# Performance work log

Measured on AMD Instinct MI355X. Metric: run time of the kernel, lower is better.

The kernel has to match this reference:

```python
import jax, jax.numpy as jnp
import numpy as np

N_NODES = 50000
N_EDGES = 600000
D = 128
LN_EPS = 1e-5


def setup_inputs() -> dict:
    key = jax.random.key(0)
    ks = jax.random.split(key, 10)
    s = 1.0 / np.sqrt(D)
    return {
        "node_reps": jax.random.normal(ks[0], (N_NODES, D), jnp.float32),
        "edge_reps": jax.random.normal(ks[1], (N_EDGES, D), jnp.float32),
        "src_idx": jax.random.randint(ks[2], (N_EDGES,), 0, N_NODES, jnp.int32),
        "dst_idx": jnp.sort(jax.random.randint(ks[3], (N_EDGES,), 0, N_NODES, jnp.int32)),
        "Wq": jax.random.normal(ks[4], (D, D), jnp.float32) * s,
        "Wk": jax.random.normal(ks[5], (D, D), jnp.float32) * s,
        "Wv": jax.random.normal(ks[6], (D, D), jnp.float32) * s,
        "Wo": jax.random.normal(ks[7], (D, D), jnp.float32) * s,
        "ln_gamma": jnp.ones((D,), jnp.float32),
        "ln_beta": jnp.zeros((D,), jnp.float32),
        "W1": jax.random.normal(ks[8], (3 * D, D), jnp.float32) * (1.0 / np.sqrt(3 * D)),
        "b1": jnp.zeros((D,), jnp.float32),
        "W2": jax.random.normal(ks[9], (D, D), jnp.float32) * s,
        "b2": jnp.zeros((D,), jnp.float32),
    }


def _layer_norm(x, g, b):
    mu = jnp.mean(x, axis=-1, keepdims=True)
    var = jnp.mean(jnp.square(x - mu), axis=-1, keepdims=True)
    return (x - mu) * jax.lax.rsqrt(var + LN_EPS) * g + b


def reference(node_reps, edge_reps, src_idx, dst_idx, Wq, Wk, Wv, Wo,
              ln_gamma, ln_beta, W1, b1, W2, b2):
    n_nodes, d = node_reps.shape
    # dense projections once per node (kernel-friendly GEMMs)
    q = node_reps @ Wq                                  # [N, d]
    k_nodes = node_reps @ Wk                            # [N, d]
    v_nodes = node_reps @ Wv                            # [N, d]
    # per-edge gather + edge bias
    k_e = k_nodes[src_idx] + edge_reps                  # [E, d]
    scores = jnp.sum(q[dst_idx] * k_e, axis=-1) / jnp.sqrt(jnp.float32(d))  # [E]
    # segment softmax over edges sharing the same dst node
    seg_max = jax.ops.segment_max(scores, dst_idx, num_segments=n_nodes)
    ex = jnp.exp(scores - seg_max[dst_idx])
    denom = jax.ops.segment_sum(ex, dst_idx, num_segments=n_nodes)
    alpha = ex / denom[dst_idx]                          # [E]
    v_e = v_nodes[src_idx] + edge_reps                   # [E, d]
    agg = jax.ops.segment_sum(alpha[:, None] * v_e, dst_idx, num_segments=n_nodes)  # [N, d]
    updated = _layer_norm(node_reps + agg @ Wo, ln_gamma, ln_beta)  # [N, d]
    # triplet fusion MLP over (dst node, edge, src node)
    h_trip = jnp.concatenate([node_reps[dst_idx], edge_reps, node_reps[src_idx]], axis=-1)  # [E, 3d]
    fused = jax.nn.relu(h_trip @ W1 + b1) @ W2 + b2      # [E, d]
    return updated, fused
```

## Files before the change

kernel.cpp:

```cpp
#include <hip/hip_runtime.h>
#include <hip/hip_bf16.h>

#define NN 50000
#define NE 600000
#define D 128

typedef __bf16 bf16x8 __attribute__((ext_vector_type(8)));
typedef __bf16 bf16x4 __attribute__((ext_vector_type(4)));
typedef float f32x4 __attribute__((ext_vector_type(4)));


static __device__ __forceinline__ void gload_lds16(const void* g, void* l) {
  __builtin_amdgcn_global_load_lds(
      (const __attribute__((address_space(1))) unsigned int*)g,
      (__attribute__((address_space(3))) unsigned int*)l, 16, 0, 0);
}

static __device__ __forceinline__ bf16x8 load_a_frag_nc(const float* __restrict__ A,
                                                        int row, int k0) {
  const f32x4* p = (const f32x4*)(A + (size_t)row * D + k0);
  f32x4 v0 = p[0], v1 = p[1];
  bf16x8 r;
  r[0] = (__bf16)v0[0]; r[1] = (__bf16)v0[1]; r[2] = (__bf16)v0[2]; r[3] = (__bf16)v0[3];
  r[4] = (__bf16)v1[0]; r[5] = (__bf16)v1[1]; r[6] = (__bf16)v1[2]; r[7] = (__bf16)v1[3];
  return r;
}

static __device__ __forceinline__ void stage_a_tile64(const float* __restrict__ A, int M,
                                                      int row_base, char* lds, int tid) {
  const int l32 = tid & 31;
  const int g = tid >> 5;
#pragma unroll
  for (int it = 0; it < 8; ++it) {
    int rl = it * 8 + g;
    int r = row_base + rl;
    f32x4 v = {};
    if (r < M) v = *(const f32x4*)(A + (size_t)r * D + l32 * 4);
    bf16x4 b;
    b[0] = (__bf16)v[0]; b[1] = (__bf16)v[1]; b[2] = (__bf16)v[2]; b[3] = (__bf16)v[3];
    int byte = (rl * 256 + l32 * 8) ^ ((rl & 7) << 4);
    *(bf16x4*)(lds + byte) = b;
  }
}

static __device__ __forceinline__ bf16x8 read_a_frag(const char* lds, int rl, int k0) {
  int byte = (rl * 256 + k0 * 2) ^ ((rl & 7) << 4);
  return *(const bf16x8*)(lds + byte);
}

template <int CTRL>
static __device__ __forceinline__ float dpp_add(float x) {
  int v = __builtin_amdgcn_update_dpp(0, __float_as_int(x), CTRL, 0xf, 0xf, true);
  return x + __int_as_float(v);
}

static __device__ __forceinline__ float red32(float x) {
  x = dpp_add<0xB1>(x);
  x = dpp_add<0x4E>(x);
  x = dpp_add<0x124>(x);
  x = dpp_add<0x128>(x);
  return x + __shfl_xor(x, 16, 64);
}

struct PrepArgs {
  const float* W[8];
  __bf16* WT[8];
  const int* dst;
  int* offs;
};

__global__ void prep_all(PrepArgs pa) {
  int b = blockIdx.x;
  if (b < 512) {
    int w = b >> 6;
    int t = (b & 63) * 256 + threadIdx.x;
    int n = t & 127, k = t >> 7;
    pa.WT[w][n * 128 + k] = (__bf16)pa.W[w][k * 128 + n];
  } else {
    int n = (b - 512) * 256 + threadIdx.x;
    if (n > NN) return;
    int lo = 0, hi = NE;
    while (lo < hi) {
      int mid = (lo + hi) >> 1;
      if (pa.dst[mid] < n) lo = mid + 1; else hi = mid;
    }
    pa.offs[n] = lo;
  }
}

struct GemmBatch {
  const __bf16* BT[5];
  void* C[5];
  const float* bias[5];
  int mode[5];
};

__global__ __launch_bounds__(256) void gemm_k128_b(const float* __restrict__ A,
                                                   GemmBatch gb, int M) {
  __shared__ __align__(16) char atile[64 * 256];
  const int tid = threadIdx.x;
  const int lane = tid & 63;
  const int wave = tid >> 6;
  const int wr = wave >> 1, wc = wave & 1;
  const int row0 = blockIdx.x * 64;
  const int col0 = wc * 64;
  const int lr = lane & 15;
  const int lk = (lane >> 4) << 3;
  const int rr = (lane >> 4) * 4;

  stage_a_tile64(A, M, row0, atile, tid);
  __syncthreads();

#pragma unroll
  for (int y = 0; y < 5; ++y) {
    const __bf16* __restrict__ BT = gb.BT[y];
    f32x4 acc[2][4] = {};
#pragma unroll
    for (int kk = 0; kk < 4; ++kk) {
      const int k0 = kk * 32 + lk;
      bf16x8 a[2], b[4];
#pragma unroll
      for (int m = 0; m < 2; ++m) a[m] = read_a_frag(atile, wr * 32 + m * 16 + lr, k0);
#pragma unroll
      for (int n = 0; n < 4; ++n) b[n] = *(const bf16x8*)(BT + (size_t)(col0 + n * 16 + lr) * D + k0);
#pragma unroll
      for (int m = 0; m < 2; ++m)
#pragma unroll
        for (int n = 0; n < 4; ++n)
          acc[m][n] = __builtin_amdgcn_mfma_f32_16x16x32_bf16(a[m], b[n], acc[m][n], 0, 0, 0);
    }
    float bv[4] = {0.f, 0.f, 0.f, 0.f};
    if (gb.bias[y]) {
#pragma unroll
      for (int n = 0; n < 4; ++n) bv[n] = gb.bias[y][col0 + n * 16 + lr];
    }
    const int mode = gb.mode[y];
#pragma unroll
    for (int m = 0; m < 2; ++m)
#pragma unroll
      for (int j = 0; j < 4; ++j) {
        const int r = row0 + wr * 32 + m * 16 + rr + j;
        if (r < M) {
#pragma unroll
          for (int n = 0; n < 4; ++n) {
            const int c = col0 + n * 16 + lr;
            const float val = acc[m][n][j] + bv[n];
            if (mode == 0) {
              ((float*)gb.C[y])[(size_t)r * D + c] = val;
            } else if (mode == 1) {
              ((__bf16*)gb.C[y])[(size_t)r * D + c] = (__bf16)val;
            } else if (mode == 2) {
              ((__bf16*)gb.C[y])[(size_t)r * 256 + c] = (__bf16)val;
            } else {
              ((__bf16*)gb.C[y])[(size_t)r * 256 + 128 + c] = (__bf16)val;
            }
          }
        }
      }
  }
}

#define LD1(P, K, J, SV)                                                     \
  do {                                                                       \
    const int jj_ = (J);                                                     \
    const int jc_ = jj_ < jm ? jj_ : 0;                                      \
    int si_ = __shfl((SV), jj_ & 31, 32);                                    \
    si_ = jj_ < jm ? si_ : 0;                                                \
    kb##P[K] = *(const bf16x4*)(KV + (size_t)si_ * 256 + (l32 << 2));        \
    vb##P[K] = *(const bf16x4*)(KV + (size_t)si_ * 256 + 128 + (l32 << 2));  \
    eb##P[K] = *(const f32x4*)(edge + (size_t)(s0 + jc_) * D + (l32 << 2));  \
  } while (0)

#define LOADC(P, C)                                                          \
  do {                                                                       \
    const int c4_ = (C) * 4;                                                 \
    const int sv_ = (c4_ < 32) ? sidx0 : sidx1;                              \
    LD1(P, 0, c4_ + 0, sv_); LD1(P, 1, c4_ + 1, sv_);                        \
    LD1(P, 2, c4_ + 2, sv_); LD1(P, 3, c4_ + 3, sv_);                        \
  } while (0)

#define CP1(P, K, J)                                                         \
  do {                                                                       \
    const int jj_ = (J);                                                     \
    f32x4 ef_ = eb##P[K];                                                    \
    float x0_ = (float)kb##P[K][0] + ef_[0];                                 \
    float x1_ = (float)kb##P[K][1] + ef_[1];                                 \
    float x2_ = (float)kb##P[K][2] + ef_[2];                                 \
    float x3_ = (float)kb##P[K][3] + ef_[3];                                 \
    float pp_ = fmaf(qs[1], x1_, qs[0] * x0_) + fmaf(qs[3], x3_, qs[2] * x2_); \
    float s_ = red32(pp_);                                                   \
    float w_ = jj_ < jm ? exp2f(s_) : 0.f;                                   \
    l += w_;                                                                 \
    a[0] = fmaf(w_, (float)vb##P[K][0] + ef_[0], a[0]);                      \
    a[1] = fmaf(w_, (float)vb##P[K][1] + ef_[1], a[1]);                      \
    a[2] = fmaf(w_, (float)vb##P[K][2] + ef_[2], a[2]);                      \
    a[3] = fmaf(w_, (float)vb##P[K][3] + ef_[3], a[3]);                      \
  } while (0)

#define COMPC(P, C)                                                          \
  do {                                                                       \
    const int cc4_ = (C) * 4;                                                \
    CP1(P, 0, cc4_ + 0); CP1(P, 1, cc4_ + 1);                                \
    CP1(P, 2, cc4_ + 2); CP1(P, 3, cc4_ + 3);                                \
  } while (0)

__global__ __launch_bounds__(256) __attribute__((amdgpu_waves_per_eu(3)))
void fused_edge_attn(
    const float* __restrict__ edge,
    const __bf16* __restrict__ W1bT,
    const __bf16* __restrict__ W2T,
    const __bf16* __restrict__ P1,
    const __bf16* __restrict__ P3,
    const int* __restrict__ dst,
    const int* __restrict__ src,
    const float* __restrict__ b2,
    float* __restrict__ out_fused,
    const float* __restrict__ Q,
    const __bf16* __restrict__ KV,
    const int* __restrict__ offs,
    const __bf16* __restrict__ WoT,
    const float* __restrict__ noderep,
    const float* __restrict__ gamma,
    const float* __restrict__ beta,
    float* __restrict__ out_updated) {
  __shared__ __align__(16) char bufA[64 * 256];
  __shared__ __align__(16) char bufB[64 * 256];
  const int tid = threadIdx.x;
  const int grp = blockIdx.x / 5;
  const int role = blockIdx.x % 5;

  if (role >= 2) {
    const int ebi = grp * 3 + (role - 2);
    const int eb = ebi * 64;
    const int lane = tid & 63;
    const int wave = tid >> 6;
    const int wr = wave >> 1, wc = wave & 1;
    const int lr = lane & 15;
    const int lk = (lane >> 4) << 3;
    const int col0 = wc * 64;

    {
      const int gr = lane >> 4;
      const int slot = lane & 15;
      int di[4], sg[4];
#pragma unroll
      for (int c = 0; c < 4; ++c) {
        int rl = wave * 16 + c * 4 + gr;
        di[c] = dst[eb + rl];
        sg[c] = src[eb + rl];
      }
#pragma unroll
      for (int c = 0; c < 4; ++c) {
        int rl = wave * 16 + c * 4 + gr;
        int sb = (slot * 16) ^ ((rl & 7) << 4);
        gload_lds16((const char*)(P1 + (size_t)di[c] * D) + sb,
                    bufA + (wave * 16 + c * 4) * 256);
        gload_lds16((const char*)(P3 + (size_t)sg[c] * D) + sb,
                    bufB + (wave * 16 + c * 4) * 256);
      }
    }

    f32x4 acc[2][4] = {};
#pragma unroll
    for (int kk = 0; kk < 4; ++kk) {
      const int k0 = kk * 32 + lk;
      bf16x8 a[2], b[4];
#pragma unroll
      for (int m = 0; m < 2; ++m) a[m] = load_a_frag_nc(edge, eb + wr * 32 + m * 16 + lr, k0);
#pragma unroll
      for (int n = 0; n < 4; ++n) b[n] = *(const bf16x8*)(W1bT + (size_t)(col0 + n * 16 + lr) * D + k0);
#pragma unroll
      for (int m = 0; m < 2; ++m)
#pragma unroll
        for (int n = 0; n < 4; ++n)
          acc[m][n] = __builtin_amdgcn_mfma_f32_16x16x32_bf16(a[m], b[n], acc[m][n], 0, 0, 0);
    }
    __syncthreads();

    const int rr = (lane >> 4) * 4;
#pragma unroll
    for (int m = 0; m < 2; ++m) {
#pragma unroll
      for (int j = 0; j < 4; ++j) {
        int rl = wr * 32 + m * 16 + rr + j;
#pragma unroll
        for (int n = 0; n < 4; ++n) {
          int c = col0 + n * 16 + lr;
          int byte = (rl * 256 + c * 2) ^ ((rl & 7) << 4);
          float g1 = (float)*(const __bf16*)(bufA + byte);
          float g3 = (float)*(const __bf16*)(bufB + byte);
          float v = fmaxf(acc[m][n][j] + g1 + g3, 0.f);
          *(__bf16*)(bufA + byte) = (__bf16)v;
        }
      }
    }
    __syncthreads();

    float b2v[4];
#pragma unroll
    for (int n = 0; n < 4; ++n) b2v[n] = b2[col0 + n * 16 + lr];
    f32x4 acc2[2][4] = {};
#pragma unroll
    for (int kk = 0; kk < 4; ++kk) {
      const int k0 = kk * 32 + lk;
      bf16x8 a[2], b[4];
#pragma unroll
      for (int m = 0; m < 2; ++m) a[m] = read_a_frag(bufA, wr * 32 + m * 16 + lr, k0);
#pragma unroll
      for (int n = 0; n < 4; ++n) b[n] = *(const bf16x8*)(W2T + (size_t)(col0 + n * 16 + lr) * D + k0);
#pragma unroll
      for (int m = 0; m < 2; ++m)
#pragma unroll
        for (int n = 0; n < 4; ++n)
          acc2[m][n] = __builtin_amdgcn_mfma_f32_16x16x32_bf16(a[m], b[n], acc2[m][n], 0, 0, 0);
    }
#pragma unroll
    for (int m = 0; m < 2; ++m)
#pragma unroll
      for (int j = 0; j < 4; ++j) {
        int rl = wr * 32 + m * 16 + rr + j;
        int e = eb + rl;
#pragma unroll
        for (int n = 0; n < 4; ++n) {
          int c = col0 + n * 16 + lr;
          out_fused[(size_t)e * D + c] = acc2[m][n][j] + b2v[n];
        }
      }
  } else {
    const int nw = tid >> 5;
    const int node = (grp * 2 + role) * 8 + nw;
    const int l32 = tid & 31;
    int s0 = offs[node], s1 = offs[node + 1];
    int cnt = s1 - s0;
    f32x4 q = *(const f32x4*)(Q + (size_t)node * D + l32 * 4);
    f32x4 qs;
    qs[0] = q[0] * 0.12751744f; qs[1] = q[1] * 0.12751744f;
    qs[2] = q[2] * 0.12751744f; qs[3] = q[3] * 0.12751744f;
    float l = 0.f;
    f32x4 a = {0.f, 0.f, 0.f, 0.f};

    const int jm = cnt < 64 ? cnt : 64;
    if (jm > 0) {
      int sidx0 = 0, sidx1 = 0;
      if (l32 < cnt) sidx0 = src[s0 + l32];
      if (l32 + 32 < cnt) sidx1 = src[s0 + 32 + l32];
      bf16x4 kb0[4], vb0[4]; f32x4 eb0[4];
      bf16x4 kb1[4], vb1[4]; f32x4 eb1[4];
      const int nch = (jm + 3) >> 2;
      LOADC(0, 0);
      for (int c = 0; c < nch; c += 2) {
        if (c + 1 < nch) LOADC(1, c + 1);
        COMPC(0, c);
        if (c + 2 < nch) LOADC(0, c + 2);
        if (c + 1 < nch) COMPC(1, c + 1);
      }
      for (int i = 64; i < cnt; ++i) {
        int si = src[s0 + i];
        bf16x4 kbx = *(const bf16x4*)(KV + (size_t)si * 256 + (l32 << 2));
        bf16x4 vbx = *(const bf16x4*)(KV + (size_t)si * 256 + 128 + (l32 << 2));
        f32x4 ef = *(const f32x4*)(edge + (size_t)(s0 + i) * D + (l32 << 2));
        float x0 = (float)kbx[0] + ef[0], x1 = (float)kbx[1] + ef[1];
        float x2 = (float)kbx[2] + ef[2], x3 = (float)kbx[3] + ef[3];
        float pp = fmaf(qs[1], x1, qs[0] * x0) + fmaf(qs[3], x3, qs[2] * x2);
        float w = exp2f(red32(pp));
        l += w;
        a[0] = fmaf(w, (float)vbx[0] + ef[0], a[0]);
        a[1] = fmaf(w, (float)vbx[1] + ef[1], a[1]);
        a[2] = fmaf(w, (float)vbx[2] + ef[2], a[2]);
        a[3] = fmaf(w, (float)vbx[3] + ef[3], a[3]);
      }
    }
    float inv = l > 0.f ? 1.f / l : 0.f;
    f32x4 r;
    r[0] = a[0] * inv; r[1] = a[1] * inv; r[2] = a[2] * inv; r[3] = a[3] * inv;

    {
      bf16x4 rb;
      rb[0] = (__bf16)r[0]; rb[1] = (__bf16)r[1];
      rb[2] = (__bf16)r[2]; rb[3] = (__bf16)r[3];
      int byte = (nw * 256 + l32 * 8) ^ ((nw & 7) << 4);
      *(bf16x4*)(bufA + byte) = rb;
    }
    __syncthreads();

    {
      const int wave = tid >> 6;
      const int lane = tid & 63;
      const int lr = lane & 15;
      const int lk = (lane >> 4) << 3;
      f32x4 acc[2] = {};
#pragma unroll
      for (int kk = 0; kk < 4; ++kk) {
        int k0 = kk * 32 + lk;
        bf16x8 af = read_a_frag(bufA, lr, k0);
#pragma unroll
        for (int t = 0; t < 2; ++t) {
          int n = wave * 2 + t;
          bf16x8 b = *(const bf16x8*)(WoT + (size_t)(n * 16 + lr) * D + k0);
          acc[t] = __builtin_amdgcn_mfma_f32_16x16x32_bf16(af, b, acc[t], 0, 0, 0);
        }
      }
      float* xl = (float*)bufB;
      const int rr = (lane >> 4) * 4;
      if (rr < 8) {
#pragma unroll
        for (int t = 0; t < 2; ++t) {
          int n = wave * 2 + t;
#pragma unroll
          for (int j = 0; j < 4; ++j)
            xl[(rr + j) * 128 + n * 16 + lr] = acc[t][j];
        }
      }
    }
    __syncthreads();

    {
      const float* xl = (const float*)bufB;
      f32x4 xv = *(const f32x4*)(xl + nw * 128 + l32 * 4);
      f32x4 nv = *(const f32x4*)(noderep + (size_t)node * D + l32 * 4);
      float x0 = xv[0] + nv[0], x1 = xv[1] + nv[1];
      float x2 = xv[2] + nv[2], x3 = xv[3] + nv[3];
      float s = red32(x0 + x1 + x2 + x3);
      float mu = s * (1.f / 128.f);
      float d0 = x0 - mu, d1 = x1 - mu, d2 = x2 - mu, d3 = x3 - mu;
      float vv = red32(d0 * d0 + d1 * d1 + d2 * d2 + d3 * d3);
      float rstd = rsqrtf(vv * (1.f / 128.f) + 1e-5f);
      f32x4 g = *(const f32x4*)(gamma + l32 * 4);
      f32x4 bb = *(const f32x4*)(beta + l32 * 4);
      f32x4 o;
      o[0] = d0 * rstd * g[0] + bb[0];
      o[1] = d1 * rstd * g[1] + bb[1];
      o[2] = d2 * rstd * g[2] + bb[2];
      o[3] = d3 * rstd * g[3] + bb[3];
      *(f32x4*)(out_updated + (size_t)node * D + l32 * 4) = o;
    }
  }
}

extern "C" void kernel_launch(void* const* d_in, const int* in_sizes, int n_in,
                              void* d_out, int out_size, void* d_ws, size_t ws_size,
                              hipStream_t stream) {
  const float* node = (const float*)d_in[0];
  const float* edge = (const float*)d_in[1];
  const int* src = (const int*)d_in[2];
  const int* dst = (const int*)d_in[3];
  const float* Wq = (const float*)d_in[4];
  const float* Wk = (const float*)d_in[5];
  const float* Wv = (const float*)d_in[6];
  const float* Wo = (const float*)d_in[7];
  const float* gamma = (const float*)d_in[8];
  const float* beta = (const float*)d_in[9];
  const float* W1 = (const float*)d_in[10];
  const float* b1 = (const float*)d_in[11];
  const float* W2 = (const float*)d_in[12];
  const float* b2 = (const float*)d_in[13];

  float* out_updated = (float*)d_out;
  float* out_fused = (float*)d_out + (size_t)NN * D;

  char* ws = (char*)d_ws;
  size_t o = 0;
  auto take = [&](size_t bytes) {
    char* p = ws + o;
    o = (o + bytes + 255) & ~(size_t)255;
    return p;
  };
  int* offs = (int*)take((NN + 1) * sizeof(int));
  __bf16* WqT = (__bf16*)take(128 * 128 * 2);
  __bf16* WkT = (__bf16*)take(128 * 128 * 2);
  __bf16* WvT = (__bf16*)take(128 * 128 * 2);
  __bf16* WoT = (__bf16*)take(128 * 128 * 2);
  __bf16* W1aT = (__bf16*)take(128 * 128 * 2);
  __bf16* W1bT = (__bf16*)take(128 * 128 * 2);
  __bf16* W1cT = (__bf16*)take(128 * 128 * 2);
  __bf16* W2T = (__bf16*)take(128 * 128 * 2);
  float* Qb = (float*)take((size_t)NN * D * 4);
  __bf16* KVb = (__bf16*)take((size_t)NN * 256 * 2);
  __bf16* P1b = (__bf16*)take((size_t)NN * D * 2);
  __bf16* P3b = (__bf16*)take((size_t)NN * D * 2);

  PrepArgs pa;
  pa.W[0] = Wq; pa.WT[0] = WqT;
  pa.W[1] = Wk; pa.WT[1] = WkT;
  pa.W[2] = Wv; pa.WT[2] = WvT;
  pa.W[3] = Wo; pa.WT[3] = WoT;
  pa.W[4] = W1; pa.WT[4] = W1aT;
  pa.W[5] = W1 + 128 * 128; pa.WT[5] = W1bT;
  pa.W[6] = W1 + 256 * 128; pa.WT[6] = W1cT;
  pa.W[7] = W2; pa.WT[7] = W2T;
  pa.dst = dst; pa.offs = offs;
  prep_all<<<512 + (NN + 256) / 256, 256, 0, stream>>>(pa);

  GemmBatch gb;
  gb.BT[0] = WqT;  gb.C[0] = Qb;  gb.bias[0] = nullptr; gb.mode[0] = 0;
  gb.BT[1] = WkT;  gb.C[1] = KVb; gb.bias[1] = nullptr; gb.mode[1] = 2;
  gb.BT[2] = WvT;  gb.C[2] = KVb; gb.bias[2] = nullptr; gb.mode[2] = 3;
  gb.BT[3] = W1aT; gb.C[3] = P1b; gb.bias[3] = b1;      gb.mode[3] = 1;
  gb.BT[4] = W1cT; gb.C[4] = P3b; gb.bias[4] = nullptr; gb.mode[4] = 1;
  gemm_k128_b<<<(NN + 63) / 64, 256, 0, stream>>>(node, gb, NN);

  fused_edge_attn<<<15625, 256, 0, stream>>>(edge, W1bT, W2T, P1b, P3b, dst, src,
                                             b2, out_fused, Qb, KVb, offs,
                                             WoT, node, gamma, beta, out_updated);
}
```

Measured before the change: 437.3 us.

## Split node GEMM over grid y, gather P1/P3 directly, interleave block roles

The node GEMM now uses 128-row tiles and assigns one of the five weight matrices to each blockIdx.y, where before every block looped over all five. The edge MLP blocks drop the LDS async gather of P1/P3 rows and read them straight from global memory in the epilogue, cutting LDS to a single buffer and raising the occupancy hint to 4 waves per EU. Block-to-role mapping is remapped in groups of 8 (with padding blocks that exit early), which interleaves attention and MLP work differently. The direct scalar bf16 global reads in the epilogue may be less coalesced than the old bulk LDS staging, and the node tile is now restaged from fp32 once per weight matrix instead of once in total.

```diff
diff --git a/kernel.cpp b/kernel.cpp
--- a/kernel.cpp
+++ b/kernel.cpp
@@ -9,12 +9,6 @@
 typedef __bf16 bf16x4 __attribute__((ext_vector_type(4)));
 typedef float f32x4 __attribute__((ext_vector_type(4)));
 
-
-static __device__ __forceinline__ void gload_lds16(const void* g, void* l) {
-  __builtin_amdgcn_global_load_lds(
-      (const __attribute__((address_space(1))) unsigned int*)g,
-      (__attribute__((address_space(3))) unsigned int*)l, 16, 0, 0);
-}
 
 static __device__ __forceinline__ bf16x8 load_a_frag_nc(const float* __restrict__ A,
                                                         int row, int k0) {
@@ -26,12 +20,12 @@
   return r;
 }
 
-static __device__ __forceinline__ void stage_a_tile64(const float* __restrict__ A, int M,
-                                                      int row_base, char* lds, int tid) {
+static __device__ __forceinline__ void stage_a_tile128(const float* __restrict__ A, int M,
+                                                       int row_base, char* lds, int tid) {
   const int l32 = tid & 31;
   const int g = tid >> 5;
 #pragma unroll
-  for (int it = 0; it < 8; ++it) {
+  for (int it = 0; it < 16; ++it) {
     int rl = it * 8 + g;
     int r = row_base + rl;
     f32x4 v = {};
@@ -97,67 +91,65 @@
 
 __global__ __launch_bounds__(256) void gemm_k128_b(const float* __restrict__ A,
                                                    GemmBatch gb, int M) {
-  __shared__ __align__(16) char atile[64 * 256];
+  __shared__ __align__(16) char atile[128 * 256];
+  const int y = blockIdx.y;
+  const __bf16* __restrict__ BT = gb.BT[y];
   const int tid = threadIdx.x;
   const int lane = tid & 63;
   const int wave = tid >> 6;
   const int wr = wave >> 1, wc = wave & 1;
-  const int row0 = blockIdx.x * 64;
+  const int row0 = blockIdx.x * 128;
   const int col0 = wc * 64;
   const int lr = lane & 15;
   const int lk = (lane >> 4) << 3;
+
+  stage_a_tile128(A, M, row0, atile, tid);
+  __syncthreads();
+
+  f32x4 acc[4][4] = {};
+#pragma unroll
+  for (int kk = 0; kk < 4; ++kk) {
+    const int k0 = kk * 32 + lk;
+    bf16x8 a[4], b[4];
+#pragma unroll
+    for (int m = 0; m < 4; ++m) a[m] = read_a_frag(atile, wr * 64 + m * 16 + lr, k0);
+#pragma unroll
+    for (int n = 0; n < 4; ++n) b[n] = *(const bf16x8*)(BT + (size_t)(col0 + n * 16 + lr) * D + k0);
+#pragma unroll
+    for (int m = 0; m < 4; ++m)
+#pragma unroll
+      for (int n = 0; n < 4; ++n)
+        acc[m][n] = __builtin_amdgcn_mfma_f32_16x16x32_bf16(a[m], b[n], acc[m][n], 0, 0, 0);
+  }
   const int rr = (lane >> 4) * 4;
-
-  stage_a_tile64(A, M, row0, atile, tid);
-  __syncthreads();
-
-#pragma unroll
-  for (int y = 0; y < 5; ++y) {
-    const __bf16* __restrict__ BT = gb.BT[y];
-    f32x4 acc[2][4] = {};
-#pragma unroll
-    for (int kk = 0; kk < 4; ++kk) {
-      const int k0 = kk * 32 + lk;
-      bf16x8 a[2], b[4];
-#pragma unroll
-      for (int m = 0; m < 2; ++m) a[m] = read_a_frag(atile, wr * 32 + m * 16 + lr, k0);
-#pragma unroll
-      for (int n = 0; n < 4; ++n) b[n] = *(const bf16x8*)(BT + (size_t)(col0 + n * 16 + lr) * D + k0);
-#pragma unroll
-      for (int m = 0; m < 2; ++m)
-#pragma unroll
-        for (int n = 0; n < 4; ++n)
-          acc[m][n] = __builtin_amdgcn_mfma_f32_16x16x32_bf16(a[m], b[n], acc[m][n], 0, 0, 0);
-    }
-    float bv[4] = {0.f, 0.f, 0.f, 0.f};
-    if (gb.bias[y]) {
-#pragma unroll
-      for (int n = 0; n < 4; ++n) bv[n] = gb.bias[y][col0 + n * 16 + lr];
-    }
-    const int mode = gb.mode[y];
-#pragma unroll
-    for (int m = 0; m < 2; ++m)
-#pragma unroll
-      for (int j = 0; j < 4; ++j) {
-        const int r = row0 + wr * 32 + m * 16 + rr + j;
-        if (r < M) {
-#pragma unroll
-          for (int n = 0; n < 4; ++n) {
-            const int c = col0 + n * 16 + lr;
-            const float val = acc[m][n][j] + bv[n];
-            if (mode == 0) {
-              ((float*)gb.C[y])[(size_t)r * D + c] = val;
-            } else if (mode == 1) {
-              ((__bf16*)gb.C[y])[(size_t)r * D + c] = (__bf16)val;
-            } else if (mode == 2) {
-              ((__bf16*)gb.C[y])[(size_t)r * 256 + c] = (__bf16)val;
-            } else {
-              ((__bf16*)gb.C[y])[(size_t)r * 256 + 128 + c] = (__bf16)val;
-            }
+  float bv[4] = {0.f, 0.f, 0.f, 0.f};
+  if (gb.bias[y]) {
+#pragma unroll
+    for (int n = 0; n < 4; ++n) bv[n] = gb.bias[y][col0 + n * 16 + lr];
+  }
+  const int mode = gb.mode[y];
+#pragma unroll
+  for (int m = 0; m < 4; ++m)
+#pragma unroll
+    for (int j = 0; j < 4; ++j) {
+      const int r = row0 + wr * 64 + m * 16 + rr + j;
+      if (r < M) {
+#pragma unroll
+        for (int n = 0; n < 4; ++n) {
+          const int c = col0 + n * 16 + lr;
+          const float val = acc[m][n][j] + bv[n];
+          if (mode == 0) {
+            ((float*)gb.C[y])[(size_t)r * D + c] = val;
+          } else if (mode == 1) {
+            ((__bf16*)gb.C[y])[(size_t)r * D + c] = (__bf16)val;
+          } else if (mode == 2) {
+            ((__bf16*)gb.C[y])[(size_t)r * 256 + c] = (__bf16)val;
+          } else {
+            ((__bf16*)gb.C[y])[(size_t)r * 256 + 128 + c] = (__bf16)val;
           }
         }
       }
-  }
+    }
 }
 
 #define LD1(P, K, J, SV)                                                     \
@@ -204,7 +196,7 @@
     CP1(P, 2, cc4_ + 2); CP1(P, 3, cc4_ + 3);                                \
   } while (0)
 
-__global__ __launch_bounds__(256) __attribute__((amdgpu_waves_per_eu(3)))
+__global__ __launch_bounds__(256) __attribute__((amdgpu_waves_per_eu(4)))
 void fused_edge_attn(
     const float* __restrict__ edge,
     const __bf16* __restrict__ W1bT,
@@ -223,11 +215,14 @@
     const float* __restrict__ gamma,
     const float* __restrict__ beta,
     float* __restrict__ out_updated) {
-  __shared__ __align__(16) char bufA[64 * 256];
-  __shared__ __align__(16) char bufB[64 * 256];
+  __shared__ __align__(16) char buf[64 * 256];
   const int tid = threadIdx.x;
-  const int grp = blockIdx.x / 5;
-  const int role = blockIdx.x % 5;
+  const int b = blockIdx.x;
+  const int x = b & 7;
+  const int t = b >> 3;
+  const int grp = (t / 5) * 8 + x;
+  const int role = t % 5;
+  if (grp >= 3125) return;
 
   if (role >= 2) {
     const int ebi = grp * 3 + (role - 2);
@@ -238,59 +233,37 @@
     const int lr = lane & 15;
     const int lk = (lane >> 4) << 3;
     const int col0 = wc * 64;
-
-    {
-      const int gr = lane >> 4;
-      const int slot = lane & 15;
-      int di[4], sg[4];
-#pragma unroll
-      for (int c = 0; c < 4; ++c) {
-        int rl = wave * 16 + c * 4 + gr;
-        di[c] = dst[eb + rl];
-        sg[c] = src[eb + rl];
-      }
-#pragma unroll
-      for (int c = 0; c < 4; ++c) {
-        int rl = wave * 16 + c * 4 + gr;
-        int sb = (slot * 16) ^ ((rl & 7) << 4);
-        gload_lds16((const char*)(P1 + (size_t)di[c] * D) + sb,
-                    bufA + (wave * 16 + c * 4) * 256);
-        gload_lds16((const char*)(P3 + (size_t)sg[c] * D) + sb,
-                    bufB + (wave * 16 + c * 4) * 256);
-      }
-    }
+    const int rr = (lane >> 4) * 4;
 
     f32x4 acc[2][4] = {};
 #pragma unroll
     for (int kk = 0; kk < 4; ++kk) {
       const int k0 = kk * 32 + lk;
-      bf16x8 a[2], b[4];
+      bf16x8 a[2], bm[4];
 #pragma unroll
       for (int m = 0; m < 2; ++m) a[m] = load_a_frag_nc(edge, eb + wr * 32 + m * 16 + lr, k0);
 #pragma unroll
-      for (int n = 0; n < 4; ++n) b[n] = *(const bf16x8*)(W1bT + (size_t)(col0 + n * 16 + lr) * D + k0);
+      for (int n = 0; n < 4; ++n) bm[n] = *(const bf16x8*)(W1bT + (size_t)(col0 + n * 16 + lr) * D + k0);
 #pragma unroll
       for (int m = 0; m < 2; ++m)
 #pragma unroll
         for (int n = 0; n < 4; ++n)
-          acc[m][n] = __builtin_amdgcn_mfma_f32_16x16x32_bf16(a[m], b[n], acc[m][n], 0, 0, 0);
-    }
-    __syncthreads();
-
-    const int rr = (lane >> 4) * 4;
+          acc[m][n] = __builtin_amdgcn_mfma_f32_16x16x32_bf16(a[m], bm[n], acc[m][n], 0, 0, 0);
+    }
+
 #pragma unroll
     for (int m = 0; m < 2; ++m) {
 #pragma unroll
       for (int j = 0; j < 4; ++j) {
-        int rl = wr * 32 + m * 16 + rr + j;
+        const int rl = wr * 32 + m * 16 + rr + j;
+        const __bf16* __restrict__ p1r = P1 + (size_t)dst[eb + rl] * D;
+        const __bf16* __restrict__ p3r = P3 + (size_t)src[eb + rl] * D;
 #pragma unroll
         for (int n = 0; n < 4; ++n) {
-          int c = col0 + n * 16 + lr;
+          const int c = col0 + n * 16 + lr;
+          float v = fmaxf(acc[m][n][j] + (float)p1r[c] + (float)p3r[c], 0.f);
           int byte = (rl * 256 + c * 2) ^ ((rl & 7) << 4);
-          float g1 = (float)*(const __bf16*)(bufA + byte);
-          float g3 = (float)*(const __bf16*)(bufB + byte);
-          float v = fmaxf(acc[m][n][j] + g1 + g3, 0.f);
-          *(__bf16*)(bufA + byte) = (__bf16)v;
+          *(__bf16*)(buf + byte) = (__bf16)v;
         }
       }
     }
@@ -303,16 +276,16 @@
 #pragma unroll
     for (int kk = 0; kk < 4; ++kk) {
       const int k0 = kk * 32 + lk;
-      bf16x8 a[2], b[4];
-#pragma unroll
-      for (int m = 0; m < 2; ++m) a[m] = read_a_frag(bufA, wr * 32 + m * 16 + lr, k0);
-#pragma unroll
-      for (int n = 0; n < 4; ++n) b[n] = *(const bf16x8*)(W2T + (size_t)(col0 + n * 16 + lr) * D + k0);
+      bf16x8 a[2], bm[4];
+#pragma unroll
+      for (int m = 0; m < 2; ++m) a[m] = read_a_frag(buf, wr * 32 + m * 16 + lr, k0);
+#pragma unroll
+      for (int n = 0; n < 4; ++n) bm[n] = *(const bf16x8*)(W2T + (size_t)(col0 + n * 16 + lr) * D + k0);
 #pragma unroll
       for (int m = 0; m < 2; ++m)
 #pragma unroll
         for (int n = 0; n < 4; ++n)
-          acc2[m][n] = __builtin_amdgcn_mfma_f32_16x16x32_bf16(a[m], b[n], acc2[m][n], 0, 0, 0);
+          acc2[m][n] = __builtin_amdgcn_mfma_f32_16x16x32_bf16(a[m], bm[n], acc2[m][n], 0, 0, 0);
     }
 #pragma unroll
     for (int m = 0; m < 2; ++m)
@@ -334,8 +307,8 @@
     int cnt = s1 - s0;
     f32x4 q = *(const f32x4*)(Q + (size_t)node * D + l32 * 4);
     f32x4 qs;
-    qs[0] = q[0] * 0.12751744f; qs[1] = q[1] * 0.12751744f;
-    qs[2] = q[2] * 0.12751744f; qs[3] = q[3] * 0.12751744f;
+    qs[0] = q[0] * 0.12751744612764933f; qs[1] = q[1] * 0.12751744612764933f;
+    qs[2] = q[2] * 0.12751744612764933f; qs[3] = q[3] * 0.12751744612764933f;
     float l = 0.f;
     f32x4 a = {0.f, 0.f, 0.f, 0.f};
 
@@ -379,7 +352,7 @@
       rb[0] = (__bf16)r[0]; rb[1] = (__bf16)r[1];
       rb[2] = (__bf16)r[2]; rb[3] = (__bf16)r[3];
       int byte = (nw * 256 + l32 * 8) ^ ((nw & 7) << 4);
-      *(bf16x4*)(bufA + byte) = rb;
+      *(bf16x4*)(buf + byte) = rb;
     }
     __syncthreads();
 
@@ -392,30 +365,30 @@
 #pragma unroll
       for (int kk = 0; kk < 4; ++kk) {
         int k0 = kk * 32 + lk;
-        bf16x8 af = read_a_frag(bufA, lr, k0);
-#pragma unroll
-        for (int t = 0; t < 2; ++t) {
-          int n = wave * 2 + t;
-          bf16x8 b = *(const bf16x8*)(WoT + (size_t)(n * 16 + lr) * D + k0);
-          acc[t] = __builtin_amdgcn_mfma_f32_16x16x32_bf16(af, b, acc[t], 0, 0, 0);
+        bf16x8 af = read_a_frag(buf, lr, k0);
+#pragma unroll
+        for (int tt = 0; tt < 2; ++tt) {
+          int nn = wave * 2 + tt;
+          bf16x8 bm = *(const bf16x8*)(WoT + (size_t)(nn * 16 + lr) * D + k0);
+          acc[tt] = __builtin_amdgcn_mfma_f32_16x16x32_bf16(af, bm, acc[tt], 0, 0, 0);
         }
       }
-      float* xl = (float*)bufB;
+      float* xl = (float*)(buf + 8192);
       const int rr = (lane >> 4) * 4;
       if (rr < 8) {
 #pragma unroll
-        for (int t = 0; t < 2; ++t) {
-          int n = wave * 2 + t;
+        for (int tt = 0; tt < 2; ++tt) {
+          int nn = wave * 2 + tt;
 #pragma unroll
           for (int j = 0; j < 4; ++j)
-            xl[(rr + j) * 128 + n * 16 + lr] = acc[t][j];
+            xl[(rr + j) * 128 + nn * 16 + lr] = acc[tt][j];
         }
       }
     }
     __syncthreads();
 
     {
-      const float* xl = (const float*)bufB;
+      const float* xl = (const float*)(buf + 8192);
       f32x4 xv = *(const f32x4*)(xl + nw * 128 + l32 * 4);
       f32x4 nv = *(const f32x4*)(noderep + (size_t)node * D + l32 * 4);
       float x0 = xv[0] + nv[0], x1 = xv[1] + nv[1];
@@ -491,15 +464,16 @@
   pa.dst = dst; pa.offs = offs;
   prep_all<<<512 + (NN + 256) / 256, 256, 0, stream>>>(pa);
 
+  int gnode = (NN + 127) / 128;
   GemmBatch gb;
   gb.BT[0] = WqT;  gb.C[0] = Qb;  gb.bias[0] = nullptr; gb.mode[0] = 0;
   gb.BT[1] = WkT;  gb.C[1] = KVb; gb.bias[1] = nullptr; gb.mode[1] = 2;
   gb.BT[2] = WvT;  gb.C[2] = KVb; gb.bias[2] = nullptr; gb.mode[2] = 3;
   gb.BT[3] = W1aT; gb.C[3] = P1b; gb.bias[3] = b1;      gb.mode[3] = 1;
   gb.BT[4] = W1cT; gb.C[4] = P3b; gb.bias[4] = nullptr; gb.mode[4] = 1;
-  gemm_k128_b<<<(NN + 63) / 64, 256, 0, stream>>>(node, gb, NN);
-
-  fused_edge_attn<<<15625, 256, 0, stream>>>(edge, W1bT, W2T, P1b, P3b, dst, src,
+  gemm_k128_b<<<dim3(gnode, 5), 256, 0, stream>>>(node, gb, NN);
+
+  fused_edge_attn<<<15640, 256, 0, stream>>>(edge, W1bT, W2T, P1b, P3b, dst, src,
                                              b2, out_fused, Qb, KVb, offs,
                                              WoT, node, gamma, beta, out_updated);
 }
```

Result: faster. 426.9 us (-2.4%).
